# Kernel tuning notes

Hardware: AMD Instinct MI355X
Metric: run time of the kernel (lower is better)

## Reference

```python
import jax, jax.numpy as jnp
import numpy as np
from jax import lax

N_EXPERTS = 8


def setup_inputs() -> dict:
    key = jax.random.key(0)
    ks = jax.random.split(key, 5)
    B, F, H, C, E = 32768, 512, 256, 100, N_EXPERTS
    x = jax.random.normal(ks[0], (B, F), dtype=jnp.float32)
    W1 = jax.random.normal(ks[1], (E, F, H), dtype=jnp.float32) * (1.0 / np.sqrt(F))
    b1 = jnp.zeros((E, H), dtype=jnp.float32)
    W2 = jax.random.normal(ks[2], (E, H, C), dtype=jnp.float32) * (1.0 / np.sqrt(H))
    b2 = jnp.zeros((E, C), dtype=jnp.float32)
    Wg = jax.random.normal(ks[3], (F, E), dtype=jnp.float32) * (1.0 / np.sqrt(F))
    return {"x": x, "W1": W1, "b1": b1, "W2": W2, "b2": b2, "Wg": Wg, "k": 2}


def reference(x, W1, b1, W2, b2, Wg, k):
    B = x.shape[0]
    # experts: per-expert 2-layer MLP, vectorized over the expert dim e
    h = jax.nn.relu(jnp.einsum('bf,efh->ebh', x, W1) + b1[:, None, :])  # [E,B,H]
    preds = jnp.einsum('ebh,ehc->ebc', h, W2) + b2[:, None, :]          # [E,B,C]
    # fixed gating: softmax over gate logits, top-k, hard 1/k weights
    probs = jax.nn.softmax(x @ Wg, axis=-1)                             # [B,E]
    _, top_idx = lax.top_k(probs, k)                                    # [B,k]
    weights = jnp.zeros_like(probs).at[jnp.arange(B)[:, None], top_idx].set(1.0 / k)
    # combined prediction: gate-weighted sum of per-expert softmaxed logits
    combined = jnp.einsum('ebc,be->bc', jax.nn.softmax(preds, axis=-1), weights)
    part_sizes = (weights > 0).sum(axis=0)  # samples routed per expert
    return combined, preds, part_sizes
```

## Files before the change

kernel.cpp:

```cpp
#include <hip/hip_runtime.h>
#include <hip/hip_bf16.h>
#include <math.h>

#define B_ 32768
#define F_ 512
#define H_ 256
#define C_ 100
#define CP 112
#define E_ 8

typedef __attribute__((ext_vector_type(8))) short bf16x8;
typedef __attribute__((ext_vector_type(4))) float f32x4;

__device__ __forceinline__ unsigned short f2b(float f) {
    unsigned int u = __float_as_uint(f);
    return (unsigned short)((u + 0x7fffu + ((u >> 16) & 1u)) >> 16);
}

__device__ __forceinline__ void gll16(const void* g, void* l) {
    __builtin_amdgcn_global_load_lds((__attribute__((address_space(1))) void*)(g),
                                     (__attribute__((address_space(3))) void*)(l),
                                     16, 0, 0);
}

__global__ __launch_bounds__(256) void k0_tr_w1(const float* __restrict__ W1,
                                                unsigned short* __restrict__ w1t) {
    __shared__ float tile[32][33];
    int e = blockIdx.z, fb = blockIdx.x * 32, hb = blockIdx.y * 32;
    int tx = threadIdx.x, ty = threadIdx.y;
    #pragma unroll
    for (int j = 0; j < 4; ++j)
        tile[ty + 8 * j][tx] = W1[((size_t)(e * F_ + fb + ty + 8 * j)) * H_ + hb + tx];
    __syncthreads();
    #pragma unroll
    for (int j = 0; j < 4; ++j)
        w1t[((size_t)(e * H_ + hb + ty + 8 * j)) * F_ + fb + tx] = f2b(tile[tx][ty + 8 * j]);
}

__global__ __launch_bounds__(256) void k0_cvt_w2(const float* __restrict__ W2,
                                                 unsigned short* __restrict__ w2t) {
    int idx = blockIdx.x * 256 + threadIdx.x;
    if (idx >= E_ * CP * H_) return;
    int e = idx / (CP * H_);
    int r = idx - e * (CP * H_);
    int c = r / H_, h = r - c * H_;
    float v = (c < C_) ? W2[((size_t)(e * H_ + h)) * C_ + c] : 0.0f;
    w2t[idx] = f2b(v);
}

__global__ __launch_bounds__(256) void k1_gate(const float* __restrict__ x,
                                               const float* __restrict__ Wg,
                                               unsigned short* __restrict__ xb,
                                               int* __restrict__ routes,
                                               float* __restrict__ part) {
    __shared__ float sWg[F_ * E_];
    __shared__ int cnt[E_];
    int tid = threadIdx.x;
    for (int i = tid; i < F_ * E_; i += 256) sWg[i] = Wg[i];
    if (tid < E_) cnt[tid] = 0;
    __syncthreads();

    int r = tid >> 3, eidx = tid & 7;
    int row = blockIdx.x * 32 + r;
    const float* xr = x + (size_t)row * F_;
    double acc = 0.0;
    for (int f = 0; f < F_; f += 4) {
        float4 xv = *(const float4*)(xr + f);
        acc += (double)xv.x * (double)sWg[(f + 0) * 8 + eidx];
        acc += (double)xv.y * (double)sWg[(f + 1) * 8 + eidx];
        acc += (double)xv.z * (double)sWg[(f + 2) * 8 + eidx];
        acc += (double)xv.w * (double)sWg[(f + 3) * 8 + eidx];
    }
    double v = acc; int ie = eidx;
    #pragma unroll
    for (int off = 1; off < 8; off <<= 1) {
        double ov = __shfl_xor(v, off);
        int oi = __shfl_xor(ie, off);
        if (ov > v || (ov == v && oi < ie)) { v = ov; ie = oi; }
    }
    int e1 = ie;
    double v2 = (eidx == e1) ? -1e300 : acc; int ie2 = eidx;
    #pragma unroll
    for (int off = 1; off < 8; off <<= 1) {
        double ov = __shfl_xor(v2, off);
        int oi = __shfl_xor(ie2, off);
        if (ov > v2 || (ov == v2 && oi < ie2)) { v2 = ov; ie2 = oi; }
    }
    int e2 = ie2;
    if (eidx == 0) {
        routes[row] = e1 | (e2 << 3);
        atomicAdd(&cnt[e1], 1);
        atomicAdd(&cnt[e2], 1);
    }
    __syncthreads();
    if (tid < E_) atomicAdd(&part[tid], (float)cnt[tid]);

    const float4* xs = (const float4*)(x + (size_t)blockIdx.x * 32 * F_);
    ushort4* xd = (ushort4*)(xb + (size_t)blockIdx.x * 32 * F_);
    #pragma unroll
    for (int i = 0; i < 16; ++i) {
        float4 xv = xs[tid + i * 256];
        ushort4 o;
        o.x = f2b(xv.x); o.y = f2b(xv.y); o.z = f2b(xv.z); o.w = f2b(xv.w);
        xd[tid + i * 256] = o;
    }
}

__global__ __launch_bounds__(256, 2) void k2_moe(const unsigned short* __restrict__ xbf,
                                                 const unsigned short* __restrict__ w1t,
                                                 const unsigned short* __restrict__ w2t,
                                                 const float* __restrict__ b1,
                                                 const float* __restrict__ b2,
                                                 float* __restrict__ preds) {
    __shared__ __align__(16) char smem[65536];
    const int tid = threadIdx.x;
    const int w = tid >> 6, lane = tid & 63;
    const int q = lane >> 4, ln = lane & 15;
    const int e = blockIdx.y;
    const int rowBase = blockIdx.x * 64;

    const int sub = lane >> 3;
    const int j8 = (lane & 7) ^ sub;
    const unsigned short* srcA0 = xbf + (size_t)(rowBase + w * 8 + sub) * F_ + 8 * j8;
    char* dstA = smem + w * 1024;
    #pragma unroll
    for (int kk = 0; kk < 8; ++kk) {
        gll16(srcA0 + kk * 64, dstA + kk * 8192);
        gll16(srcA0 + 32 * F_ + kk * 64, dstA + kk * 8192 + 4096);
    }

    float bias1[4];
    #pragma unroll
    for (int nt = 0; nt < 4; ++nt) bias1[nt] = b1[e * H_ + w * 64 + nt * 16 + ln];

    f32x4 acc[4][4];
    #pragma unroll
    for (int i = 0; i < 4; ++i)
        #pragma unroll
        for (int j = 0; j < 4; ++j) acc[i][j] = (f32x4){0.f, 0.f, 0.f, 0.f};

    const unsigned short* bb = w1t + ((size_t)e * H_ + w * 64 + ln) * F_ + q * 8;
    bf16x8 bcur[4], bnxt[4];
    #pragma unroll
    for (int nt = 0; nt < 4; ++nt) bcur[nt] = *(const bf16x8*)(bb + nt * 16 * F_);

    __syncthreads();

    #pragma unroll
    for (int h = 0; h < 16; ++h) {
        const int kk = h >> 1, ks = h & 1;
        if (h < 15) {
            const int off2 = ((h + 1) >> 1) * 64 + ((h + 1) & 1) * 32;
            #pragma unroll
            for (int nt = 0; nt < 4; ++nt)
                bnxt[nt] = *(const bf16x8*)(bb + nt * 16 * F_ + off2);
        }
        const int slot = ((ks * 4 + q) ^ (ln & 7)) * 16;
        bf16x8 af[4];
        #pragma unroll
        for (int mt = 0; mt < 4; ++mt)
            af[mt] = *(const bf16x8*)(smem + kk * 8192 + (mt * 16 + ln) * 128 + slot);
        #pragma unroll
        for (int mt = 0; mt < 4; ++mt)
            #pragma unroll
            for (int nt = 0; nt < 4; ++nt)
                acc[mt][nt] = __builtin_amdgcn_mfma_f32_16x16x32_bf16(af[mt], bcur[nt], acc[mt][nt], 0, 0, 0);
        #pragma unroll
        for (int nt = 0; nt < 4; ++nt) bcur[nt] = bnxt[nt];
    }

    __syncthreads();

    const unsigned short* w2base = w2t + ((size_t)e * CP + ln) * H_ + q * 8;
    bf16x8 wreg[2][7];
    #pragma unroll
    for (int mt = 0; mt < 7; ++mt)
        wreg[0][mt] = *(const bf16x8*)(w2base + mt * 16 * H_);

    #pragma unroll
    for (int mt = 0; mt < 4; ++mt)
        #pragma unroll
        for (int nt = 0; nt < 4; ++nt)
            #pragma unroll
            for (int r2 = 0; r2 < 4; ++r2) {
                int rr = mt * 16 + q * 4 + r2;
                int col = w * 64 + nt * 16 + ln;
                float v = fmaxf(acc[mt][nt][r2] + bias1[nt], 0.0f);
                *(unsigned short*)(smem + rr * 528 + col * 2) = f2b(v);
            }

    f32x4 acc2[7];
    #pragma unroll
    for (int i = 0; i < 7; ++i) acc2[i] = (f32x4){0.f, 0.f, 0.f, 0.f};
    const int offH = (w * 16 + ln) * 528 + q * 16;

    __syncthreads();

    #pragma unroll
    for (int kc = 0; kc < 8; ++kc) {
        const int cur = kc & 1, nxt = cur ^ 1;
        if (kc < 7) {
            #pragma unroll
            for (int mt = 0; mt < 7; ++mt)
                wreg[nxt][mt] = *(const bf16x8*)(w2base + mt * 16 * H_ + (kc + 1) * 32);
        }
        bf16x8 hb = *(const bf16x8*)(smem + offH + kc * 64);
        #pragma unroll
        for (int mt = 0; mt < 7; ++mt)
            acc2[mt] = __builtin_amdgcn_mfma_f32_16x16x32_bf16(wreg[cur][mt], hb, acc2[mt], 0, 0, 0);
    }

    int row = rowBase + w * 16 + ln;
    #pragma unroll
    for (int mt = 0; mt < 7; ++mt) {
        int c0 = mt * 16 + q * 4;
        if (c0 + 3 < C_) {
            f32x4 bias = *(const f32x4*)(b2 + e * C_ + c0);
            f32x4 o = acc2[mt] + bias;
            *(f32x4*)(preds + ((size_t)e * B_ + row) * C_ + c0) = o;
        }
    }
}

__global__ __launch_bounds__(256) void k3_combine(const float* __restrict__ preds,
                                                  const int* __restrict__ routes,
                                                  float* __restrict__ combined) {
    __shared__ float pbuf[4][104];
    int tid = threadIdx.x, wv = tid >> 6, lane = tid & 63;
    int row = blockIdx.x * 2 + (wv >> 1);
    int rt = routes[row];
    int e = (wv & 1) ? ((rt >> 3) & 7) : (rt & 7);
    const float* pr = preds + ((size_t)e * B_ + row) * C_;
    float a0 = (lane < C_) ? pr[lane] : -1e30f;
    float a1 = (lane + 64 < C_) ? pr[lane + 64] : -1e30f;
    float m = fmaxf(a0, a1);
    #pragma unroll
    for (int off = 32; off; off >>= 1) m = fmaxf(m, __shfl_xor(m, off));
    float s0 = (lane < C_) ? expf(a0 - m) : 0.f;
    float s1 = (lane + 64 < C_) ? expf(a1 - m) : 0.f;
    float s = s0 + s1;
    #pragma unroll
    for (int off = 32; off; off >>= 1) s += __shfl_xor(s, off);
    float inv = 0.5f / s;
    if (lane < C_) pbuf[wv][lane] = s0 * inv;
    if (lane + 64 < C_) pbuf[wv][lane + 64] = s1 * inv;
    __syncthreads();
    if (tid < C_)
        combined[(size_t)(blockIdx.x * 2) * C_ + tid] = pbuf[0][tid] + pbuf[1][tid];
    else if (tid >= 128 && tid < 128 + C_)
        combined[(size_t)(blockIdx.x * 2 + 1) * C_ + (tid - 128)] = pbuf[2][tid - 128] + pbuf[3][tid - 128];
}

extern "C" void kernel_launch(void* const* d_in, const int* in_sizes, int n_in,
                              void* d_out, int out_size, void* d_ws, size_t ws_size,
                              hipStream_t stream) {
    (void)in_sizes; (void)n_in; (void)out_size;
    const float* x  = (const float*)d_in[0];
    const float* W1 = (const float*)d_in[1];
    const float* b1 = (const float*)d_in[2];
    const float* W2 = (const float*)d_in[3];
    const float* b2 = (const float*)d_in[4];
    const float* Wg = (const float*)d_in[5];

    float* out = (float*)d_out;
    float* combined = out;
    float* preds = out + (size_t)B_ * C_;
    float* part  = out + (size_t)B_ * C_ + (size_t)E_ * B_ * C_;

    char* ws = (char*)d_ws;
    unsigned short* xbf = (unsigned short*)ws;
    unsigned short* w1t = (unsigned short*)(ws + 33554432);
    unsigned short* w2t = (unsigned short*)(ws + 35651584);
    int* routes = (int*)(ws + 36110336);
    if (ws_size < 36241408) return;

    hipMemsetAsync(part, 0, E_ * sizeof(float), stream);
    k0_tr_w1<<<dim3(F_ / 32, H_ / 32, E_), dim3(32, 8), 0, stream>>>(W1, w1t);
    k0_cvt_w2<<<(E_ * CP * H_ + 255) / 256, 256, 0, stream>>>(W2, w2t);
    k1_gate<<<B_ / 32, 256, 0, stream>>>(x, Wg, xbf, routes, part);
    k2_moe<<<dim3(B_ / 64, E_), 256, 0, stream>>>(xbf, w1t, w2t, b1, b2, preds);
    k3_combine<<<B_ / 2, 256, 0, stream>>>(preds, routes, combined);
}
```

Baseline: 460.5 us.

## Fuse expert loop and combine softmax into single MoE kernel

The MoE kernel now loops over all 8 experts inside one block, reusing the x tile loaded into LDS once instead of reloading it per expert. It computes the per-expert softmax and the gate-weighted combine in registers, which removes the separate combine kernel and its re-read of preds. The hidden activations are staged through a smaller swizzled LDS buffer in two halves. In exchange the grid shrinks eightfold (512 blocks), LDS grows to 80KB, and there are more barriers per block, which may reduce occupancy and parallelism.

```diff
diff --git a/kernel.cpp b/kernel.cpp
--- a/kernel.cpp
+++ b/kernel.cpp
@@ -111,12 +111,13 @@
                                                  const unsigned short* __restrict__ w2t,
                                                  const float* __restrict__ b1,
                                                  const float* __restrict__ b2,
-                                                 float* __restrict__ preds) {
-    __shared__ __align__(16) char smem[65536];
+                                                 const int* __restrict__ routes,
+                                                 float* __restrict__ preds,
+                                                 float* __restrict__ combined) {
+    __shared__ __align__(16) char smem[81920];
     const int tid = threadIdx.x;
     const int w = tid >> 6, lane = tid & 63;
     const int q = lane >> 4, ln = lane & 15;
-    const int e = blockIdx.y;
     const int rowBase = blockIdx.x * 64;
 
     const int sub = lane >> 3;
@@ -129,126 +130,178 @@
         gll16(srcA0 + 32 * F_ + kk * 64, dstA + kk * 8192 + 4096);
     }
 
-    float bias1[4];
-    #pragma unroll
-    for (int nt = 0; nt < 4; ++nt) bias1[nt] = b1[e * H_ + w * 64 + nt * 16 + ln];
-
-    f32x4 acc[4][4];
-    #pragma unroll
-    for (int i = 0; i < 4; ++i)
-        #pragma unroll
-        for (int j = 0; j < 4; ++j) acc[i][j] = (f32x4){0.f, 0.f, 0.f, 0.f};
-
-    const unsigned short* bb = w1t + ((size_t)e * H_ + w * 64 + ln) * F_ + q * 8;
-    bf16x8 bcur[4], bnxt[4];
-    #pragma unroll
-    for (int nt = 0; nt < 4; ++nt) bcur[nt] = *(const bf16x8*)(bb + nt * 16 * F_);
+    const int lrow = w * 16 + ln;
+    const int row = rowBase + lrow;
+    const int rt = routes[row];
+
+    const unsigned short* bb = w1t + (size_t)(w * 64 + ln) * F_ + q * 8;
+    bf16x8 bc[2][4], bn[2][4];
+    #pragma unroll
+    for (int ks2 = 0; ks2 < 2; ++ks2)
+        #pragma unroll
+        for (int nt = 0; nt < 4; ++nt)
+            bc[ks2][nt] = *(const bf16x8*)(bb + nt * 16 * F_ + ks2 * 32);
+
+    f32x4 comb[7];
+    #pragma unroll
+    for (int mt = 0; mt < 7; ++mt) comb[mt] = (f32x4){0.f, 0.f, 0.f, 0.f};
+
+    const unsigned short* w2b = w2t + (size_t)ln * H_ + q * 8;
 
     __syncthreads();
 
-    #pragma unroll
-    for (int h = 0; h < 16; ++h) {
-        const int kk = h >> 1, ks = h & 1;
-        if (h < 15) {
-            const int off2 = ((h + 1) >> 1) * 64 + ((h + 1) & 1) * 32;
-            #pragma unroll
-            for (int nt = 0; nt < 4; ++nt)
-                bnxt[nt] = *(const bf16x8*)(bb + nt * 16 * F_ + off2);
-        }
-        const int slot = ((ks * 4 + q) ^ (ln & 7)) * 16;
-        bf16x8 af[4];
+    for (int e = 0; e < E_; ++e) {
+        float bias1[4];
+        #pragma unroll
+        for (int nt = 0; nt < 4; ++nt) bias1[nt] = b1[e * H_ + w * 64 + nt * 16 + ln];
+
+        f32x4 acc[4][4];
+        #pragma unroll
+        for (int i = 0; i < 4; ++i)
+            #pragma unroll
+            for (int j = 0; j < 4; ++j) acc[i][j] = (f32x4){0.f, 0.f, 0.f, 0.f};
+
+        #pragma unroll
+        for (int kk = 0; kk < 8; ++kk) {
+            const size_t pfo = (kk < 7) ? (size_t)(kk + 1) * 64
+                                        : ((e < E_ - 1) ? (size_t)H_ * F_ : 0);
+            const unsigned short* pf = bb + pfo;
+            #pragma unroll
+            for (int ks2 = 0; ks2 < 2; ++ks2)
+                #pragma unroll
+                for (int nt = 0; nt < 4; ++nt)
+                    bn[ks2][nt] = *(const bf16x8*)(pf + nt * 16 * F_ + ks2 * 32);
+            #pragma unroll
+            for (int ks = 0; ks < 2; ++ks) {
+                const int slot = ((ks * 4 + q) ^ (ln & 7)) * 16;
+                bf16x8 af[4];
+                #pragma unroll
+                for (int mt = 0; mt < 4; ++mt)
+                    af[mt] = *(const bf16x8*)(smem + kk * 8192 + (mt * 16 + ln) * 128 + slot);
+                #pragma unroll
+                for (int mt = 0; mt < 4; ++mt)
+                    #pragma unroll
+                    for (int nt = 0; nt < 4; ++nt)
+                        acc[mt][nt] = __builtin_amdgcn_mfma_f32_16x16x32_bf16(af[mt], bc[ks][nt], acc[mt][nt], 0, 0, 0);
+            }
+            #pragma unroll
+            for (int ks2 = 0; ks2 < 2; ++ks2)
+                #pragma unroll
+                for (int nt = 0; nt < 4; ++nt)
+                    bc[ks2][nt] = bn[ks2][nt];
+        }
+        bb += (size_t)H_ * F_;
+
+        bf16x8 wv[2][7];
+        #pragma unroll
+        for (int mt = 0; mt < 7; ++mt)
+            wv[0][mt] = *(const bf16x8*)(w2b + mt * 16 * H_);
+
+        __syncthreads();
+
         #pragma unroll
         for (int mt = 0; mt < 4; ++mt)
-            af[mt] = *(const bf16x8*)(smem + kk * 8192 + (mt * 16 + ln) * 128 + slot);
+            #pragma unroll
+            for (int nt2 = 0; nt2 < 2; ++nt2)
+                #pragma unroll
+                for (int r2 = 0; r2 < 4; ++r2) {
+                    int rr = mt * 16 + q * 4 + r2;
+                    int hp = w * 32 + nt2 * 16 + ln;
+                    float v = fmaxf(acc[mt][nt2][r2] + bias1[nt2], 0.0f);
+                    *(unsigned short*)(smem + 65536 + rr * 256 +
+                                       (((hp >> 3) ^ (rr & 15)) << 4) + ((hp & 7) << 1)) = f2b(v);
+                }
+        __syncthreads();
+
+        f32x4 acc2[7];
+        #pragma unroll
+        for (int mt = 0; mt < 7; ++mt) acc2[mt] = (f32x4){0.f, 0.f, 0.f, 0.f};
+
+        #pragma unroll
+        for (int j = 0; j < 4; ++j) {
+            const int nc = (j < 3) ? (2 * (j + 1)) * 32 : 32;
+            #pragma unroll
+            for (int mt = 0; mt < 7; ++mt)
+                wv[(j + 1) & 1][mt] = *(const bf16x8*)(w2b + mt * 16 * H_ + nc);
+            bf16x8 hb = *(const bf16x8*)(smem + 65536 + lrow * 256 + (((4 * j + q) ^ ln) << 4));
+            #pragma unroll
+            for (int mt = 0; mt < 7; ++mt)
+                acc2[mt] = __builtin_amdgcn_mfma_f32_16x16x32_bf16(wv[j & 1][mt], hb, acc2[mt], 0, 0, 0);
+        }
+        __syncthreads();
+
         #pragma unroll
         for (int mt = 0; mt < 4; ++mt)
             #pragma unroll
-            for (int nt = 0; nt < 4; ++nt)
-                acc[mt][nt] = __builtin_amdgcn_mfma_f32_16x16x32_bf16(af[mt], bcur[nt], acc[mt][nt], 0, 0, 0);
-        #pragma unroll
-        for (int nt = 0; nt < 4; ++nt) bcur[nt] = bnxt[nt];
-    }
-
-    __syncthreads();
-
-    const unsigned short* w2base = w2t + ((size_t)e * CP + ln) * H_ + q * 8;
-    bf16x8 wreg[2][7];
-    #pragma unroll
-    for (int mt = 0; mt < 7; ++mt)
-        wreg[0][mt] = *(const bf16x8*)(w2base + mt * 16 * H_);
-
-    #pragma unroll
-    for (int mt = 0; mt < 4; ++mt)
-        #pragma unroll
-        for (int nt = 0; nt < 4; ++nt)
-            #pragma unroll
-            for (int r2 = 0; r2 < 4; ++r2) {
-                int rr = mt * 16 + q * 4 + r2;
-                int col = w * 64 + nt * 16 + ln;
-                float v = fmaxf(acc[mt][nt][r2] + bias1[nt], 0.0f);
-                *(unsigned short*)(smem + rr * 528 + col * 2) = f2b(v);
+            for (int nt2 = 2; nt2 < 4; ++nt2)
+                #pragma unroll
+                for (int r2 = 0; r2 < 4; ++r2) {
+                    int rr = mt * 16 + q * 4 + r2;
+                    int hp = w * 32 + (nt2 - 2) * 16 + ln;
+                    float v = fmaxf(acc[mt][nt2][r2] + bias1[nt2], 0.0f);
+                    *(unsigned short*)(smem + 65536 + rr * 256 +
+                                       (((hp >> 3) ^ (rr & 15)) << 4) + ((hp & 7) << 1)) = f2b(v);
+                }
+        __syncthreads();
+
+        #pragma unroll
+        for (int j = 0; j < 4; ++j) {
+            if (j < 3) {
+                const int nc = (2 * (j + 1) + 1) * 32;
+                #pragma unroll
+                for (int mt = 0; mt < 7; ++mt)
+                    wv[(j + 1) & 1][mt] = *(const bf16x8*)(w2b + mt * 16 * H_ + nc);
             }
-
-    f32x4 acc2[7];
-    #pragma unroll
-    for (int i = 0; i < 7; ++i) acc2[i] = (f32x4){0.f, 0.f, 0.f, 0.f};
-    const int offH = (w * 16 + ln) * 528 + q * 16;
-
-    __syncthreads();
-
-    #pragma unroll
-    for (int kc = 0; kc < 8; ++kc) {
-        const int cur = kc & 1, nxt = cur ^ 1;
-        if (kc < 7) {
+            bf16x8 hb = *(const bf16x8*)(smem + 65536 + lrow * 256 + (((4 * j + q) ^ ln) << 4));
             #pragma unroll
             for (int mt = 0; mt < 7; ++mt)
-                wreg[nxt][mt] = *(const bf16x8*)(w2base + mt * 16 * H_ + (kc + 1) * 32);
-        }
-        bf16x8 hb = *(const bf16x8*)(smem + offH + kc * 64);
-        #pragma unroll
-        for (int mt = 0; mt < 7; ++mt)
-            acc2[mt] = __builtin_amdgcn_mfma_f32_16x16x32_bf16(wreg[cur][mt], hb, acc2[mt], 0, 0, 0);
-    }
-
-    int row = rowBase + w * 16 + ln;
+                acc2[mt] = __builtin_amdgcn_mfma_f32_16x16x32_bf16(wv[j & 1][mt], hb, acc2[mt], 0, 0, 0);
+        }
+        w2b += (size_t)CP * H_;
+
+        float mx = -1e30f;
+        #pragma unroll
+        for (int mt = 0; mt < 7; ++mt) {
+            const int c0 = mt * 16 + q * 4;
+            if (c0 + 3 < C_) {
+                f32x4 bias = *(const f32x4*)(b2 + e * C_ + c0);
+                acc2[mt] += bias;
+                *(f32x4*)(preds + ((size_t)e * B_ + row) * C_ + c0) = acc2[mt];
+                #pragma unroll
+                for (int r2 = 0; r2 < 4; ++r2) mx = fmaxf(mx, acc2[mt][r2]);
+            }
+        }
+        mx = fmaxf(mx, __shfl_xor(mx, 16));
+        mx = fmaxf(mx, __shfl_xor(mx, 32));
+        float s = 0.f;
+        #pragma unroll
+        for (int mt = 0; mt < 7; ++mt) {
+            const int c0 = mt * 16 + q * 4;
+            if (c0 + 3 < C_) {
+                #pragma unroll
+                for (int r2 = 0; r2 < 4; ++r2) {
+                    acc2[mt][r2] = __expf(acc2[mt][r2] - mx);
+                    s += acc2[mt][r2];
+                }
+            }
+        }
+        s += __shfl_xor(s, 16);
+        s += __shfl_xor(s, 32);
+        const float fac = 0.5f * ((((rt & 7) == e) ? 1.f : 0.f) +
+                                  ((((rt >> 3) & 7) == e) ? 1.f : 0.f)) / s;
+        #pragma unroll
+        for (int mt = 0; mt < 7; ++mt) {
+            const int c0 = mt * 16 + q * 4;
+            if (c0 + 3 < C_) comb[mt] += acc2[mt] * fac;
+        }
+    }
+
     #pragma unroll
     for (int mt = 0; mt < 7; ++mt) {
-        int c0 = mt * 16 + q * 4;
-        if (c0 + 3 < C_) {
-            f32x4 bias = *(const f32x4*)(b2 + e * C_ + c0);
-            f32x4 o = acc2[mt] + bias;
-            *(f32x4*)(preds + ((size_t)e * B_ + row) * C_ + c0) = o;
-        }
-    }
-}
-
-__global__ __launch_bounds__(256) void k3_combine(const float* __restrict__ preds,
-                                                  const int* __restrict__ routes,
-                                                  float* __restrict__ combined) {
-    __shared__ float pbuf[4][104];
-    int tid = threadIdx.x, wv = tid >> 6, lane = tid & 63;
-    int row = blockIdx.x * 2 + (wv >> 1);
-    int rt = routes[row];
-    int e = (wv & 1) ? ((rt >> 3) & 7) : (rt & 7);
-    const float* pr = preds + ((size_t)e * B_ + row) * C_;
-    float a0 = (lane < C_) ? pr[lane] : -1e30f;
-    float a1 = (lane + 64 < C_) ? pr[lane + 64] : -1e30f;
-    float m = fmaxf(a0, a1);
-    #pragma unroll
-    for (int off = 32; off; off >>= 1) m = fmaxf(m, __shfl_xor(m, off));
-    float s0 = (lane < C_) ? expf(a0 - m) : 0.f;
-    float s1 = (lane + 64 < C_) ? expf(a1 - m) : 0.f;
-    float s = s0 + s1;
-    #pragma unroll
-    for (int off = 32; off; off >>= 1) s += __shfl_xor(s, off);
-    float inv = 0.5f / s;
-    if (lane < C_) pbuf[wv][lane] = s0 * inv;
-    if (lane + 64 < C_) pbuf[wv][lane + 64] = s1 * inv;
-    __syncthreads();
-    if (tid < C_)
-        combined[(size_t)(blockIdx.x * 2) * C_ + tid] = pbuf[0][tid] + pbuf[1][tid];
-    else if (tid >= 128 && tid < 128 + C_)
-        combined[(size_t)(blockIdx.x * 2 + 1) * C_ + (tid - 128)] = pbuf[2][tid - 128] + pbuf[3][tid - 128];
+        const int c0 = mt * 16 + q * 4;
+        if (c0 + 3 < C_)
+            *(f32x4*)(combined + (size_t)row * C_ + c0) = comb[mt];
+    }
 }
 
 extern "C" void kernel_launch(void* const* d_in, const int* in_sizes, int n_in,
@@ -278,6 +331,5 @@
     k0_tr_w1<<<dim3(F_ / 32, H_ / 32, E_), dim3(32, 8), 0, stream>>>(W1, w1t);
     k0_cvt_w2<<<(E_ * CP * H_ + 255) / 256, 256, 0, stream>>>(W2, w2t);
     k1_gate<<<B_ / 32, 256, 0, stream>>>(x, Wg, xbf, routes, part);
-    k2_moe<<<dim3(B_ / 64, E_), 256, 0, stream>>>(xbf, w1t, w2t, b1, b2, preds);
-    k3_combine<<<B_ / 2, 256, 0, stream>>>(preds, routes, combined);
-}
+    k2_moe<<<dim3(B_ / 64), 256, 0, stream>>>(xbf, w1t, w2t, b1, b2, routes, preds, combined);
+}
```

New measurement: 437.0 us. 1.05x faster.

## Loop over experts inside block to reuse staged x tile across all experts

Applied to the files above, without the earlier changes.

The MoE kernel now launches one 512-thread block per 128 rows and loops over all 8 experts inside the block. The x tile is loaded into LDS once and reused for every expert, instead of being reloaded by 8 separate expert blocks. The second GEMM splits W2 output columns across 8 waves, uses a padded 128-column W2 and an XOR-swizzled hidden buffer, and processes the two 64-row halves in turn. The cost is 160KB of LDS per block, which likely allows only one block per CU, plus serialized expert iterations with several barriers each, so latency hiding may suffer.

```diff
diff --git a/kernel.cpp b/kernel.cpp
--- a/kernel.cpp
+++ b/kernel.cpp
@@ -6,7 +6,7 @@
 #define F_ 512
 #define H_ 256
 #define C_ 100
-#define CP 112
+#define CP2 128
 #define E_ 8
 
 typedef __attribute__((ext_vector_type(8))) short bf16x8;
@@ -40,9 +40,9 @@
 __global__ __launch_bounds__(256) void k0_cvt_w2(const float* __restrict__ W2,
                                                  unsigned short* __restrict__ w2t) {
     int idx = blockIdx.x * 256 + threadIdx.x;
-    if (idx >= E_ * CP * H_) return;
-    int e = idx / (CP * H_);
-    int r = idx - e * (CP * H_);
+    if (idx >= E_ * CP2 * H_) return;
+    int e = idx / (CP2 * H_);
+    int r = idx - e * (CP2 * H_);
     int c = r / H_, h = r - c * H_;
     float v = (c < C_) ? W2[((size_t)(e * H_ + h)) * C_ + c] : 0.0f;
     w2t[idx] = f2b(v);
@@ -106,118 +106,166 @@
     }
 }
 
-__global__ __launch_bounds__(256, 2) void k2_moe(const unsigned short* __restrict__ xbf,
+__global__ __launch_bounds__(512, 2) void k2_moe(const unsigned short* __restrict__ xbf,
                                                  const unsigned short* __restrict__ w1t,
                                                  const unsigned short* __restrict__ w2t,
                                                  const float* __restrict__ b1,
                                                  const float* __restrict__ b2,
                                                  float* __restrict__ preds) {
-    __shared__ __align__(16) char smem[65536];
+    __shared__ __align__(16) char smem[163840];
+    char* sH = smem + 131072;
     const int tid = threadIdx.x;
     const int w = tid >> 6, lane = tid & 63;
     const int q = lane >> 4, ln = lane & 15;
-    const int e = blockIdx.y;
-    const int rowBase = blockIdx.x * 64;
+    const int mg = w >> 2;
+    const int ng = w & 3;
+    const int rowBase = blockIdx.x * 128;
 
     const int sub = lane >> 3;
     const int j8 = (lane & 7) ^ sub;
-    const unsigned short* srcA0 = xbf + (size_t)(rowBase + w * 8 + sub) * F_ + 8 * j8;
-    char* dstA = smem + w * 1024;
+    const unsigned short* srcA0 = xbf + (size_t)(rowBase + mg * 64 + ng * 8 + sub) * F_ + 8 * j8;
+    char* dstA = smem + mg * 65536 + ng * 1024;
     #pragma unroll
     for (int kk = 0; kk < 8; ++kk) {
         gll16(srcA0 + kk * 64, dstA + kk * 8192);
         gll16(srcA0 + 32 * F_ + kk * 64, dstA + kk * 8192 + 4096);
     }
 
-    float bias1[4];
-    #pragma unroll
-    for (int nt = 0; nt < 4; ++nt) bias1[nt] = b1[e * H_ + w * 64 + nt * 16 + ln];
-
-    f32x4 acc[4][4];
-    #pragma unroll
-    for (int i = 0; i < 4; ++i)
-        #pragma unroll
-        for (int j = 0; j < 4; ++j) acc[i][j] = (f32x4){0.f, 0.f, 0.f, 0.f};
-
-    const unsigned short* bb = w1t + ((size_t)e * H_ + w * 64 + ln) * F_ + q * 8;
-    bf16x8 bcur[4], bnxt[4];
-    #pragma unroll
-    for (int nt = 0; nt < 4; ++nt) bcur[nt] = *(const bf16x8*)(bb + nt * 16 * F_);
-
-    __syncthreads();
-
-    #pragma unroll
-    for (int h = 0; h < 16; ++h) {
-        const int kk = h >> 1, ks = h & 1;
-        if (h < 15) {
-            const int off2 = ((h + 1) >> 1) * 64 + ((h + 1) & 1) * 32;
-            #pragma unroll
-            for (int nt = 0; nt < 4; ++nt)
-                bnxt[nt] = *(const bf16x8*)(bb + nt * 16 * F_ + off2);
-        }
-        const int slot = ((ks * 4 + q) ^ (ln & 7)) * 16;
-        bf16x8 af[4];
-        #pragma unroll
-        for (int mt = 0; mt < 4; ++mt)
-            af[mt] = *(const bf16x8*)(smem + kk * 8192 + (mt * 16 + ln) * 128 + slot);
-        #pragma unroll
-        for (int mt = 0; mt < 4; ++mt)
-            #pragma unroll
-            for (int nt = 0; nt < 4; ++nt)
-                acc[mt][nt] = __builtin_amdgcn_mfma_f32_16x16x32_bf16(af[mt], bcur[nt], acc[mt][nt], 0, 0, 0);
-        #pragma unroll
-        for (int nt = 0; nt < 4; ++nt) bcur[nt] = bnxt[nt];
-    }
-
-    __syncthreads();
-
-    const unsigned short* w2base = w2t + ((size_t)e * CP + ln) * H_ + q * 8;
-    bf16x8 wreg[2][7];
-    #pragma unroll
-    for (int mt = 0; mt < 7; ++mt)
-        wreg[0][mt] = *(const bf16x8*)(w2base + mt * 16 * H_);
-
-    #pragma unroll
-    for (int mt = 0; mt < 4; ++mt)
+    const unsigned short* bb = w1t + (size_t)(ng * 64 + ln) * F_ + q * 8;
+    bf16x8 bc[2][4], bn[2][4];
+    #pragma unroll
+    for (int ks2 = 0; ks2 < 2; ++ks2)
         #pragma unroll
         for (int nt = 0; nt < 4; ++nt)
-            #pragma unroll
-            for (int r2 = 0; r2 < 4; ++r2) {
-                int rr = mt * 16 + q * 4 + r2;
-                int col = w * 64 + nt * 16 + ln;
-                float v = fmaxf(acc[mt][nt][r2] + bias1[nt], 0.0f);
-                *(unsigned short*)(smem + rr * 528 + col * 2) = f2b(v);
+            bc[ks2][nt] = *(const bf16x8*)(bb + nt * 16 * F_ + ks2 * 32);
+
+    __syncthreads();
+
+    for (int e = 0; e < E_; ++e) {
+        float bias1[4];
+        #pragma unroll
+        for (int nt = 0; nt < 4; ++nt) bias1[nt] = b1[e * H_ + ng * 64 + nt * 16 + ln];
+
+        f32x4 acc[4][4];
+        #pragma unroll
+        for (int i = 0; i < 4; ++i)
+            #pragma unroll
+            for (int j = 0; j < 4; ++j) acc[i][j] = (f32x4){0.f, 0.f, 0.f, 0.f};
+
+        #pragma unroll
+        for (int kk = 0; kk < 8; ++kk) {
+            const size_t pfo = (kk < 7) ? (size_t)(kk + 1) * 64
+                                        : ((e < E_ - 1) ? (size_t)H_ * F_ : 0);
+            const unsigned short* pf = bb + pfo;
+            #pragma unroll
+            for (int ks2 = 0; ks2 < 2; ++ks2)
+                #pragma unroll
+                for (int nt = 0; nt < 4; ++nt)
+                    bn[ks2][nt] = *(const bf16x8*)(pf + nt * 16 * F_ + ks2 * 32);
+            #pragma unroll
+            for (int ks = 0; ks < 2; ++ks) {
+                const int slot = ((ks * 4 + q) ^ (ln & 7)) * 16;
+                bf16x8 af[4];
+                #pragma unroll
+                for (int mt = 0; mt < 4; ++mt)
+                    af[mt] = *(const bf16x8*)(smem + mg * 65536 + kk * 8192 + (mt * 16 + ln) * 128 + slot);
+                #pragma unroll
+                for (int mt = 0; mt < 4; ++mt)
+                    #pragma unroll
+                    for (int nt = 0; nt < 4; ++nt)
+                        acc[mt][nt] = __builtin_amdgcn_mfma_f32_16x16x32_bf16(af[mt], bc[ks][nt], acc[mt][nt], 0, 0, 0);
             }
-
-    f32x4 acc2[7];
-    #pragma unroll
-    for (int i = 0; i < 7; ++i) acc2[i] = (f32x4){0.f, 0.f, 0.f, 0.f};
-    const int offH = (w * 16 + ln) * 528 + q * 16;
-
-    __syncthreads();
-
-    #pragma unroll
-    for (int kc = 0; kc < 8; ++kc) {
-        const int cur = kc & 1, nxt = cur ^ 1;
-        if (kc < 7) {
-            #pragma unroll
-            for (int mt = 0; mt < 7; ++mt)
-                wreg[nxt][mt] = *(const bf16x8*)(w2base + mt * 16 * H_ + (kc + 1) * 32);
-        }
-        bf16x8 hb = *(const bf16x8*)(smem + offH + kc * 64);
-        #pragma unroll
-        for (int mt = 0; mt < 7; ++mt)
-            acc2[mt] = __builtin_amdgcn_mfma_f32_16x16x32_bf16(wreg[cur][mt], hb, acc2[mt], 0, 0, 0);
-    }
-
-    int row = rowBase + w * 16 + ln;
-    #pragma unroll
-    for (int mt = 0; mt < 7; ++mt) {
-        int c0 = mt * 16 + q * 4;
-        if (c0 + 3 < C_) {
-            f32x4 bias = *(const f32x4*)(b2 + e * C_ + c0);
-            f32x4 o = acc2[mt] + bias;
-            *(f32x4*)(preds + ((size_t)e * B_ + row) * C_ + c0) = o;
+            #pragma unroll
+            for (int ks2 = 0; ks2 < 2; ++ks2)
+                #pragma unroll
+                for (int nt = 0; nt < 4; ++nt)
+                    bc[ks2][nt] = bn[ks2][nt];
+        }
+        bb += (size_t)H_ * F_;
+
+        const unsigned short* w2s = w2t + ((size_t)(e * CP2 + w * 16 + ln)) * H_ + q * 8;
+        bf16x8 wv[8];
+        #pragma unroll
+        for (int kc = 0; kc < 8; ++kc)
+            wv[kc] = *(const bf16x8*)(w2s + kc * 32);
+
+        const int c0 = w * 16 + q * 4;
+        f32x4 b2f = (f32x4){0.f, 0.f, 0.f, 0.f};
+        if (c0 + 3 < C_) b2f = *(const f32x4*)(b2 + e * C_ + c0);
+
+        __syncthreads();
+
+        if (mg == 0) {
+            #pragma unroll
+            for (int mt = 0; mt < 4; ++mt)
+                #pragma unroll
+                for (int nt = 0; nt < 4; ++nt)
+                    #pragma unroll
+                    for (int r2 = 0; r2 < 4; ++r2) {
+                        int rr = mt * 16 + q * 4 + r2;
+                        int hp = ng * 64 + nt * 16 + ln;
+                        float v = fmaxf(acc[mt][nt][r2] + bias1[nt], 0.0f);
+                        *(unsigned short*)(sH + rr * 512 + ((((hp >> 3) ^ (rr & 31)) << 4)) + ((hp & 7) << 1)) = f2b(v);
+                    }
+        }
+        __syncthreads();
+
+        {
+            f32x4 acc2[4];
+            #pragma unroll
+            for (int nt = 0; nt < 4; ++nt) acc2[nt] = (f32x4){0.f, 0.f, 0.f, 0.f};
+            #pragma unroll
+            for (int kc = 0; kc < 8; ++kc)
+                #pragma unroll
+                for (int nt = 0; nt < 4; ++nt) {
+                    const int r16 = nt * 16 + ln;
+                    bf16x8 hb = *(const bf16x8*)(sH + r16 * 512 + ((((kc * 4 + q) ^ (r16 & 31)) << 4)));
+                    acc2[nt] = __builtin_amdgcn_mfma_f32_16x16x32_bf16(wv[kc], hb, acc2[nt], 0, 0, 0);
+                }
+            if (c0 + 3 < C_) {
+                #pragma unroll
+                for (int nt = 0; nt < 4; ++nt) {
+                    int row = rowBase + nt * 16 + ln;
+                    *(f32x4*)(preds + ((size_t)e * B_ + row) * C_ + c0) = acc2[nt] + b2f;
+                }
+            }
+        }
+        __syncthreads();
+
+        if (mg == 1) {
+            #pragma unroll
+            for (int mt = 0; mt < 4; ++mt)
+                #pragma unroll
+                for (int nt = 0; nt < 4; ++nt)
+                    #pragma unroll
+                    for (int r2 = 0; r2 < 4; ++r2) {
+                        int rr = mt * 16 + q * 4 + r2;
+                        int hp = ng * 64 + nt * 16 + ln;
+                        float v = fmaxf(acc[mt][nt][r2] + bias1[nt], 0.0f);
+                        *(unsigned short*)(sH + rr * 512 + ((((hp >> 3) ^ (rr & 31)) << 4)) + ((hp & 7) << 1)) = f2b(v);
+                    }
+        }
+        __syncthreads();
+
+        {
+            f32x4 acc2[4];
+            #pragma unroll
+            for (int nt = 0; nt < 4; ++nt) acc2[nt] = (f32x4){0.f, 0.f, 0.f, 0.f};
+            #pragma unroll
+            for (int kc = 0; kc < 8; ++kc)
+                #pragma unroll
+                for (int nt = 0; nt < 4; ++nt) {
+                    const int r16 = nt * 16 + ln;
+                    bf16x8 hb = *(const bf16x8*)(sH + r16 * 512 + ((((kc * 4 + q) ^ (r16 & 31)) << 4)));
+                    acc2[nt] = __builtin_amdgcn_mfma_f32_16x16x32_bf16(wv[kc], hb, acc2[nt], 0, 0, 0);
+                }
+            if (c0 + 3 < C_) {
+                #pragma unroll
+                for (int nt = 0; nt < 4; ++nt) {
+                    int row = rowBase + 64 + nt * 16 + ln;
+                    *(f32x4*)(preds + ((size_t)e * B_ + row) * C_ + c0) = acc2[nt] + b2f;
+                }
+            }
         }
     }
 }
@@ -271,13 +319,13 @@
     unsigned short* xbf = (unsigned short*)ws;
     unsigned short* w1t = (unsigned short*)(ws + 33554432);
     unsigned short* w2t = (unsigned short*)(ws + 35651584);
-    int* routes = (int*)(ws + 36110336);
-    if (ws_size < 36241408) return;
+    int* routes = (int*)(ws + 36175872);
+    if (ws_size < 36306944) return;
 
     hipMemsetAsync(part, 0, E_ * sizeof(float), stream);
     k0_tr_w1<<<dim3(F_ / 32, H_ / 32, E_), dim3(32, 8), 0, stream>>>(W1, w1t);
-    k0_cvt_w2<<<(E_ * CP * H_ + 255) / 256, 256, 0, stream>>>(W2, w2t);
+    k0_cvt_w2<<<(E_ * CP2 * H_ + 255) / 256, 256, 0, stream>>>(W2, w2t);
     k1_gate<<<B_ / 32, 256, 0, stream>>>(x, Wg, xbf, routes, part);
-    k2_moe<<<dim3(B_ / 64, E_), 256, 0, stream>>>(xbf, w1t, w2t, b1, b2, preds);
+    k2_moe<<<dim3(B_ / 128), 512, 0, stream>>>(xbf, w1t, w2t, b1, b2, preds);
     k3_combine<<<B_ / 2, 256, 0, stream>>>(preds, routes, combined);
 }
```

New measurement: 455.7 us. No clear change (-1.0%).
